# Performance work log

Measured on AMD Instinct MI355X. Metric: run time of the kernel, lower is better.

Reference implementation:

```python
import jax, jax.numpy as jnp
import numpy as np

N, D_IN, D_OUT = 8192, 256, 64
NEG_INF = -9e15
LEAKY_SLOPE = 0.2  # tf.nn.leaky_relu default alpha


def setup_inputs() -> dict:
    key = jax.random.key(0)
    k1, k2, k3, k4 = jax.random.split(key, 4)
    x = jax.random.normal(k1, (N, D_IN), dtype=jnp.float32)
    adj = jax.random.randint(k2, (N, N), 0, 2, dtype=jnp.int32)
    W = jax.random.normal(k3, (D_IN, D_OUT), dtype=jnp.float32) * (1.0 / np.sqrt(D_IN))
    a = jax.random.normal(k4, (2 * D_OUT, 1), dtype=jnp.float32) * (1.0 / np.sqrt(2 * D_OUT))
    b = jnp.zeros((D_OUT,), dtype=jnp.float32)
    return {"x": x, "adj": adj, "W": W, "a": a, "b": b}


def reference(x, adj, W, a, b):
    # z: [N, D_OUT]
    z = x @ W
    # Additive GAT scores: e[i,j] = leaky_relu(a1.z_i + a2.z_j)
    # (equivalent to the tile/concat + matmul with a in the original,
    #  but avoids the [N*N, 2D] intermediate)
    a1 = a[:D_OUT, 0]   # [D_OUT]
    a2 = a[D_OUT:, 0]   # [D_OUT]
    si = z @ a1         # [N]
    sj = z @ a2         # [N]
    e = jax.nn.leaky_relu(si[:, None] + sj[None, :], negative_slope=LEAKY_SLOPE)
    masked = jnp.where(adj > 0, e, NEG_INF)
    alpha = jax.nn.softmax(masked, axis=1)  # row-wise over neighbors
    out = alpha @ z + b
    return jax.nn.relu(out)
```

## Files before the change

### kernel.cpp

```cpp
#include <hip/hip_runtime.h>
#include <hip/hip_bf16.h>

#define N 8192
#define DIN 256
#define DOUT 64
#define JSPLIT 32
#define JSPAN (N / JSPLIT)
#define KSTEPS (JSPAN / 32)
#define NITILES (N / 64)
#define LEAKY 0.2f

typedef __attribute__((ext_vector_type(8))) short bf16x8;
typedef __attribute__((ext_vector_type(4))) float f32x4;

#define OFF_ZT   ((size_t)0)
#define OFF_SI   (OFF_ZT + (size_t)DOUT * N * 2)
#define OFF_SJ   (OFF_SI + (size_t)N * 4)
#define OFF_MAX  (OFF_SJ + (size_t)N * 4)
#define OFF_PDEN (OFF_MAX + 256)
#define OFF_PNUM (OFF_PDEN + (size_t)JSPLIT * N * 4)

static __device__ __forceinline__ short f2bf(float f) {
  union { __hip_bfloat16 h; short s; } u;
  u.h = __float2bfloat16(f);
  return u.s;
}

static __device__ __forceinline__ unsigned fkey(float f) {
  int b = __float_as_int(f);
  return (b < 0) ? ~(unsigned)b : ((unsigned)b | 0x80000000u);
}
static __device__ __forceinline__ float fdec(unsigned k) {
  int b = (k & 0x80000000u) ? (int)(k & 0x7fffffffu) : (int)~k;
  return __int_as_float(b);
}

__global__ __launch_bounds__(256) void gat_proj(
    const float* __restrict__ x, const float* __restrict__ W,
    const float* __restrict__ a, __hip_bfloat16* __restrict__ zT,
    float* __restrict__ si, float* __restrict__ sj,
    unsigned* __restrict__ mx) {
  __shared__ float wmx[4][2];
  const int lane = threadIdx.x & 63;
  const int wave = threadIdx.x >> 6;
  const int rowbase = blockIdx.x * 16 + wave * 4;
  float acc[4] = {0.f, 0.f, 0.f, 0.f};
  for (int k = 0; k < DIN; k += 4) {
    const float w0 = W[(k + 0) * DOUT + lane];
    const float w1 = W[(k + 1) * DOUT + lane];
    const float w2 = W[(k + 2) * DOUT + lane];
    const float w3 = W[(k + 3) * DOUT + lane];
#pragma unroll
    for (int r = 0; r < 4; ++r) {
      const float4 xv = *reinterpret_cast<const float4*>(&x[(size_t)(rowbase + r) * DIN + k]);
      acc[r] += xv.x * w0 + xv.y * w1 + xv.z * w2 + xv.w * w3;
    }
  }
  const float a1l = a[lane];
  const float a2l = a[DOUT + lane];
  float wm1 = -1e30f, wm2 = -1e30f;
#pragma unroll
  for (int r = 0; r < 4; ++r) {
    const int row = rowbase + r;
    zT[(size_t)lane * N + row] = __float2bfloat16(acc[r]);
    float v1 = acc[r] * a1l;
    float v2 = acc[r] * a2l;
#pragma unroll
    for (int m = 1; m < 64; m <<= 1) {
      v1 += __shfl_xor(v1, m);
      v2 += __shfl_xor(v2, m);
    }
    if (lane == 0) { si[row] = v1; sj[row] = v2; }
    wm1 = fmaxf(wm1, v1);
    wm2 = fmaxf(wm2, v2);
  }
  if (lane == 0) { wmx[wave][0] = wm1; wmx[wave][1] = wm2; }
  __syncthreads();
  if (threadIdx.x == 0) {
    float M1 = fmaxf(fmaxf(wmx[0][0], wmx[1][0]), fmaxf(wmx[2][0], wmx[3][0]));
    float M2 = fmaxf(fmaxf(wmx[0][1], wmx[1][1]), fmaxf(wmx[2][1], wmx[3][1]));
    atomicMax(mx + 0, fkey(M1));
    atomicMax(mx + 1, fkey(M2));
  }
}

__global__ __launch_bounds__(256, 4) void gat_main(
    const int* __restrict__ adj, const float* __restrict__ si,
    const float* __restrict__ sj, const __hip_bfloat16* __restrict__ zT,
    const unsigned* __restrict__ mx, float* __restrict__ pnum,
    float* __restrict__ pden) {
  __shared__ short lds_z[64][264];
  const int tid = threadIdx.x;
  const int lane = tid & 63;
  const int wave = tid >> 6;
  const int itile = blockIdx.x % NITILES;
  const int jchunk = blockIdx.x / NITILES;
  const int r16 = lane & 15;
  const int kgrp = lane >> 4;
  const int row = itile * 64 + wave * 16 + r16;
  const int jbase = jchunk * JSPAN;

  {
    const int r = tid >> 5;
    const int cb = (tid & 31) * 8;
#pragma unroll
    for (int rr = 0; rr < 8; ++rr) {
      const int d = rr * 8 + r;
      const bf16x8 v =
          *reinterpret_cast<const bf16x8*>(zT + (size_t)d * N + jbase + cb);
      *reinterpret_cast<bf16x8*>(&lds_z[d][cb]) = v;
    }
  }

  unsigned bm0 = 0, bm1 = 0;
  {
    const int* __restrict__ abase =
        adj + (size_t)(itile * 64 + wave * 16) * N + jbase;
#pragma unroll
    for (int rr = 0; rr < 16; ++rr) {
#pragma unroll
      for (int w = 0; w < 4; ++w) {
        const int v = abase[(size_t)rr * N + w * 64 + lane];
        const unsigned long long m = __ballot(v > 0);
        const unsigned byte0 = (unsigned)(m >> (kgrp * 8)) & 0xffu;
        const unsigned byte1 = (unsigned)(m >> (32 + kgrp * 8)) & 0xffu;
        const unsigned contrib = (byte0 | (byte1 << 8)) << ((w & 1) * 16);
        if (r16 == rr) {
          if (w < 2) bm0 |= contrib; else bm1 |= contrib;
        }
      }
    }
  }
  __syncthreads();

  const float tC = fdec(mx[0]) + fdec(mx[1]);
  const float C = tC > 0.f ? tC : LEAKY * tC;
  const float sir = si[row];
  const float* __restrict__ sp = sj + jbase + kgrp * 8;

  f32x4 acc0 = {0.f, 0.f, 0.f, 0.f};
  f32x4 acc1 = acc0, acc2 = acc0, acc3 = acc0;
  float dacc = 0.f;

#pragma unroll
  for (int it = 0; it < KSTEPS; ++it) {
    const unsigned bmp = (it < 4) ? bm0 : bm1;
    const unsigned bits = (bmp >> ((it & 3) * 8)) & 0xffu;
    const int col = it * 32 + kgrp * 8;

    const bf16x8 b0 = *reinterpret_cast<const bf16x8*>(&lds_z[r16][col]);
    const bf16x8 b1 = *reinterpret_cast<const bf16x8*>(&lds_z[16 + r16][col]);
    const bf16x8 b2 = *reinterpret_cast<const bf16x8*>(&lds_z[32 + r16][col]);
    const bf16x8 b3 = *reinterpret_cast<const bf16x8*>(&lds_z[48 + r16][col]);
    const float4 s0 = *reinterpret_cast<const float4*>(sp + it * 32);
    const float4 s1 = *reinterpret_cast<const float4*>(sp + it * 32 + 4);

    float p0, p1, p2, p3, p4, p5, p6, p7, t;
    t = sir + s0.x; t = fmaxf(t, LEAKY * t); p0 = (bits & 1u)   ? __expf(t - C) : 0.f;
    t = sir + s0.y; t = fmaxf(t, LEAKY * t); p1 = (bits & 2u)   ? __expf(t - C) : 0.f;
    t = sir + s0.z; t = fmaxf(t, LEAKY * t); p2 = (bits & 4u)   ? __expf(t - C) : 0.f;
    t = sir + s0.w; t = fmaxf(t, LEAKY * t); p3 = (bits & 8u)   ? __expf(t - C) : 0.f;
    t = sir + s1.x; t = fmaxf(t, LEAKY * t); p4 = (bits & 16u)  ? __expf(t - C) : 0.f;
    t = sir + s1.y; t = fmaxf(t, LEAKY * t); p5 = (bits & 32u)  ? __expf(t - C) : 0.f;
    t = sir + s1.z; t = fmaxf(t, LEAKY * t); p6 = (bits & 64u)  ? __expf(t - C) : 0.f;
    t = sir + s1.w; t = fmaxf(t, LEAKY * t); p7 = (bits & 128u) ? __expf(t - C) : 0.f;

    dacc += ((p0 + p1) + (p2 + p3)) + ((p4 + p5) + (p6 + p7));

    bf16x8 afr;
    afr[0] = f2bf(p0); afr[1] = f2bf(p1); afr[2] = f2bf(p2); afr[3] = f2bf(p3);
    afr[4] = f2bf(p4); afr[5] = f2bf(p5); afr[6] = f2bf(p6); afr[7] = f2bf(p7);

    acc0 = __builtin_amdgcn_mfma_f32_16x16x32_bf16(afr, b0, acc0, 0, 0, 0);
    acc1 = __builtin_amdgcn_mfma_f32_16x16x32_bf16(afr, b1, acc1, 0, 0, 0);
    acc2 = __builtin_amdgcn_mfma_f32_16x16x32_bf16(afr, b2, acc2, 0, 0, 0);
    acc3 = __builtin_amdgcn_mfma_f32_16x16x32_bf16(afr, b3, acc3, 0, 0, 0);
  }

  dacc += __shfl_xor(dacc, 16);
  dacc += __shfl_xor(dacc, 32);
  if (lane < 16) pden[(size_t)jchunk * N + row] = dacc;

  float* np = pnum + ((size_t)jchunk * N + (size_t)itile * 64 + wave * 16) * DOUT;
  const f32x4 accs[4] = {acc0, acc1, acc2, acc3};
#pragma unroll
  for (int dt = 0; dt < 4; ++dt) {
#pragma unroll
    for (int r = 0; r < 4; ++r) {
      np[(kgrp * 4 + r) * DOUT + dt * 16 + r16] = accs[dt][r];
    }
  }
}

__global__ __launch_bounds__(256) void gat_combine(
    const float* __restrict__ pnum, const float* __restrict__ pden,
    const float* __restrict__ b, float* __restrict__ out) {
  const int idx = blockIdx.x * 256 + threadIdx.x;
  const int row = idx >> 6;
  const int d = idx & 63;
  float num = 0.f, den = 0.f;
#pragma unroll
  for (int s = 0; s < JSPLIT; ++s) num += pnum[(size_t)s * N * DOUT + idx];
#pragma unroll
  for (int s = 0; s < JSPLIT; ++s) den += pden[(size_t)s * N + row];
  const float o = num / den + b[d];
  out[idx] = o > 0.f ? o : 0.f;
}

extern "C" void kernel_launch(void* const* d_in, const int* in_sizes, int n_in,
                              void* d_out, int out_size, void* d_ws, size_t ws_size,
                              hipStream_t stream) {
  const float* x = (const float*)d_in[0];
  const int* adj = (const int*)d_in[1];
  const float* W = (const float*)d_in[2];
  const float* a = (const float*)d_in[3];
  const float* b = (const float*)d_in[4];
  float* out = (float*)d_out;
  char* ws = (char*)d_ws;

  __hip_bfloat16* zT = (__hip_bfloat16*)(ws + OFF_ZT);
  float* si = (float*)(ws + OFF_SI);
  float* sj = (float*)(ws + OFF_SJ);
  unsigned* mx = (unsigned*)(ws + OFF_MAX);
  float* pden = (float*)(ws + OFF_PDEN);
  float* pnum = (float*)(ws + OFF_PNUM);

  gat_proj<<<dim3(N / 16), dim3(256), 0, stream>>>(x, W, a, zT, si, sj, mx);
  gat_main<<<dim3(NITILES * JSPLIT), dim3(256), 0, stream>>>(adj, si, sj, zT, mx,
                                                             pnum, pden);
  gat_combine<<<dim3((N * DOUT) / 256), dim3(256), 0, stream>>>(pnum, pden, b, out);
}
```

Measured before the change: 438.4 us.

## Batch adjacency loads, XOR-swizzle LDS z tile, raise occupancy hint

```diff
diff --git a/kernel.cpp b/kernel.cpp
--- a/kernel.cpp
+++ b/kernel.cpp
@@ -84,12 +84,12 @@
   }
 }
 
-__global__ __launch_bounds__(256, 4) void gat_main(
+__global__ __launch_bounds__(256, 5) void gat_main(
     const int* __restrict__ adj, const float* __restrict__ si,
     const float* __restrict__ sj, const __hip_bfloat16* __restrict__ zT,
     const unsigned* __restrict__ mx, float* __restrict__ pnum,
     float* __restrict__ pden) {
-  __shared__ short lds_z[64][264];
+  __shared__ short lds_z[64][256];
   const int tid = threadIdx.x;
   const int lane = tid & 63;
   const int wave = tid >> 6;
@@ -101,34 +101,46 @@
   const int jbase = jchunk * JSPAN;
 
   {
-    const int r = tid >> 5;
-    const int cb = (tid & 31) * 8;
+    const int rgrp = tid >> 5;
+    const int cslot = (tid & 31) * 16;
+    char* ldsb = (char*)&lds_z[0][0];
 #pragma unroll
     for (int rr = 0; rr < 8; ++rr) {
-      const int d = rr * 8 + r;
-      const bf16x8 v =
-          *reinterpret_cast<const bf16x8*>(zT + (size_t)d * N + jbase + cb);
-      *reinterpret_cast<bf16x8*>(&lds_z[d][cb]) = v;
+      const int d = rr * 8 + rgrp;
+      const bf16x8 v = *reinterpret_cast<const bf16x8*>(
+          zT + (size_t)d * N + jbase + (tid & 31) * 8);
+      *reinterpret_cast<bf16x8*>(ldsb + d * 512 + (cslot ^ ((d & 7) << 4))) = v;
     }
   }
 
   unsigned bm0 = 0, bm1 = 0;
+  const int* __restrict__ abase =
+      adj + (size_t)(itile * 64 + wave * 16) * N + jbase;
   {
-    const int* __restrict__ abase =
-        adj + (size_t)(itile * 64 + wave * 16) * N + jbase;
-#pragma unroll
-    for (int rr = 0; rr < 16; ++rr) {
-#pragma unroll
-      for (int w = 0; w < 4; ++w) {
-        const int v = abase[(size_t)rr * N + w * 64 + lane];
-        const unsigned long long m = __ballot(v > 0);
-        const unsigned byte0 = (unsigned)(m >> (kgrp * 8)) & 0xffu;
-        const unsigned byte1 = (unsigned)(m >> (32 + kgrp * 8)) & 0xffu;
-        const unsigned contrib = (byte0 | (byte1 << 8)) << ((w & 1) * 16);
-        if (r16 == rr) {
-          if (w < 2) bm0 |= contrib; else bm1 |= contrib;
-        }
-      }
+    int va[32];
+#pragma unroll
+    for (int i = 0; i < 32; ++i)
+      va[i] = abase[(size_t)(i >> 2) * N + (i & 3) * 64 + lane];
+#pragma unroll
+    for (int i = 0; i < 32; ++i) {
+      const int rr = i >> 2, w = i & 3;
+      const unsigned long long m = __ballot(va[i] > 0);
+      const unsigned b0 = (unsigned)(m >> (kgrp * 8)) & 0xffu;
+      const unsigned b1 = (unsigned)(m >> (32 + kgrp * 8)) & 0xffu;
+      const unsigned contrib = (b0 | (b1 << 8)) << ((w & 1) * 16);
+      if (r16 == rr) { if (w < 2) bm0 |= contrib; else bm1 |= contrib; }
+    }
+#pragma unroll
+    for (int i = 0; i < 32; ++i)
+      va[i] = abase[(size_t)(8 + (i >> 2)) * N + (i & 3) * 64 + lane];
+#pragma unroll
+    for (int i = 0; i < 32; ++i) {
+      const int rr = 8 + (i >> 2), w = i & 3;
+      const unsigned long long m = __ballot(va[i] > 0);
+      const unsigned b0 = (unsigned)(m >> (kgrp * 8)) & 0xffu;
+      const unsigned b1 = (unsigned)(m >> (32 + kgrp * 8)) & 0xffu;
+      const unsigned contrib = (b0 | (b1 << 8)) << ((w & 1) * 16);
+      if (r16 == rr) { if (w < 2) bm0 |= contrib; else bm1 |= contrib; }
     }
   }
   __syncthreads();
@@ -137,6 +149,8 @@
   const float C = tC > 0.f ? tC : LEAKY * tC;
   const float sir = si[row];
   const float* __restrict__ sp = sj + jbase + kgrp * 8;
+  const char* __restrict__ zr0 = (const char*)&lds_z[0][0] + r16 * 512;
+  const int swz = (r16 & 7) << 4;
 
   f32x4 acc0 = {0.f, 0.f, 0.f, 0.f};
   f32x4 acc1 = acc0, acc2 = acc0, acc3 = acc0;
@@ -144,14 +158,13 @@
 
 #pragma unroll
   for (int it = 0; it < KSTEPS; ++it) {
-    const unsigned bmp = (it < 4) ? bm0 : bm1;
-    const unsigned bits = (bmp >> ((it & 3) * 8)) & 0xffu;
-    const int col = it * 32 + kgrp * 8;
-
-    const bf16x8 b0 = *reinterpret_cast<const bf16x8*>(&lds_z[r16][col]);
-    const bf16x8 b1 = *reinterpret_cast<const bf16x8*>(&lds_z[16 + r16][col]);
-    const bf16x8 b2 = *reinterpret_cast<const bf16x8*>(&lds_z[32 + r16][col]);
-    const bf16x8 b3 = *reinterpret_cast<const bf16x8*>(&lds_z[48 + r16][col]);
+    const unsigned bits = ((it < 4 ? bm0 : bm1) >> ((it & 3) * 8)) & 0xffu;
+    const int cb = (it * 64 + kgrp * 16) ^ swz;
+
+    const bf16x8 b0 = *reinterpret_cast<const bf16x8*>(zr0 + cb);
+    const bf16x8 b1 = *reinterpret_cast<const bf16x8*>(zr0 + 16 * 512 + cb);
+    const bf16x8 b2 = *reinterpret_cast<const bf16x8*>(zr0 + 32 * 512 + cb);
+    const bf16x8 b3 = *reinterpret_cast<const bf16x8*>(zr0 + 48 * 512 + cb);
     const float4 s0 = *reinterpret_cast<const float4*>(sp + it * 32);
     const float4 s1 = *reinterpret_cast<const float4*>(sp + it * 32 + 4);
 
```

Measured after the change: 429.6 us. -2.0%, faster.
